# Kernel optimization log

Measured on AMD Instinct MI355X. Metric: run time of the kernel, lower is better.

The kernel has to match this reference:

```python
import jax, jax.numpy as jnp
import numpy as np

# Config (matches init_kwargs)
B, DIM = 16, 768
HEADS, DHEAD = 12, 64
H_MEM, W_MEM = 16, 16           # memory grid; N = 256 tokens
MAX_AH, MAX_AW = 3, 3
N = H_MEM * W_MEM


def _area_pool(t):
    """t: [B', N, D] laid out on an H_MEM x W_MEM grid.
    Returns (area_sums [B', M, D], area_sizes [M]) over all rectangle sizes
    (ah, aw) with 1<=ah<=MAX_AH, 1<=aw<=MAX_AW, at every valid position,
    via a 2D integral image (summed-area table)."""
    Bp, _, D = t.shape
    g = t.reshape(Bp, H_MEM, W_MEM, D)
    I = jnp.cumsum(jnp.cumsum(g, axis=1), axis=2)
    I = jnp.pad(I, ((0, 0), (1, 0), (1, 0), (0, 0)))  # [B', H+1, W+1, D]
    sums, sizes = [], []
    for ah in range(1, MAX_AH + 1):
        for aw in range(1, MAX_AW + 1):
            s = (I[:, ah:, aw:] - I[:, :-ah, aw:]
                 - I[:, ah:, :-aw] + I[:, :-ah, :-aw])  # [B', H-ah+1, W-aw+1, D]
            n_pos = s.shape[1] * s.shape[2]
            sums.append(s.reshape(Bp, n_pos, D))
            sizes.append(np.full((n_pos,), float(ah * aw), dtype=np.float32))
    return jnp.concatenate(sums, axis=1), jnp.asarray(np.concatenate(sizes))


def setup_inputs() -> dict:
    key = jax.random.key(0)
    ks = jax.random.split(key, 10)
    s = 0.02
    d = dict(
        x=jax.random.normal(ks[0], (B, N, DIM), jnp.float32),
        # to_qkv: Linear(dim, 3*dim, bias=False); stored as (in, out)
        w_qkv=jax.random.normal(ks[1], (DIM, 3 * DIM), jnp.float32) * s,
        # per-head q/k/v projections (dim -> heads*dim_head) with bias
        w_q=jax.random.normal(ks[2], (DIM, HEADS * DHEAD), jnp.float32) * s,
        b_q=jnp.zeros((HEADS * DHEAD,), jnp.float32),
        w_k=jax.random.normal(ks[3], (DIM, HEADS * DHEAD), jnp.float32) * s,
        b_k=jnp.zeros((HEADS * DHEAD,), jnp.float32),
        w_v=jax.random.normal(ks[4], (DIM, HEADS * DHEAD), jnp.float32) * s,
        b_v=jnp.zeros((HEADS * DHEAD,), jnp.float32),
        # output projection (heads*dim_head -> dim)
        w_o=jax.random.normal(ks[5], (HEADS * DHEAD, DIM), jnp.float32) * s,
        b_o=jnp.zeros((DIM,), jnp.float32),
    )
    return d


def reference(x, w_qkv, w_q, b_q, w_k, b_k, w_v, b_v, w_o, b_o):
    # QKV projection + split: 'b n (qkv d) -> qkv b n d'
    qkv = x @ w_qkv                               # [B, N, 3*DIM]
    q, k, v = jnp.split(qkv, 3, axis=-1)          # each [B, N, DIM]

    def to_heads(t, w, b):                        # 'b n (h d) -> (b h) n d'
        return ((t @ w + b)
                .reshape(B, N, HEADS, DHEAD)
                .transpose(0, 2, 1, 3)
                .reshape(B * HEADS, N, DHEAD))

    qh = to_heads(q, w_q, b_q)
    kh = to_heads(k, w_k, b_k)
    vh = to_heads(v, w_v, b_v)

    # Area keys: mean over each area; area values: sum over each area.
    k_sum, sizes = _area_pool(kh)                 # [BH, M, d], [M]
    k_area = k_sum / sizes[None, :, None]
    v_area, _ = _area_pool(vh)                    # [BH, M, d]

    logits = jnp.einsum('bqd,bmd->bqm', qh, k_area)   # [BH, N, M]
    weights = jax.nn.softmax(logits, axis=-1)
    out = jnp.einsum('bqm,bmd->bqd', weights, v_area)  # [BH, N, d]

    # '(b h) n d -> b n (h d)' then output projection
    out = (out.reshape(B, HEADS, N, DHEAD)
              .transpose(0, 2, 1, 3)
              .reshape(B, N, HEADS * DHEAD))
    return out @ w_o + b_o
```

## Files before the change

kernel.cpp:

```cpp
#include <hip/hip_runtime.h>
#include <hip/hip_bf16.h>

typedef __hip_bfloat16 bf16;
typedef __attribute__((ext_vector_type(8))) short short8b;
typedef __attribute__((ext_vector_type(4))) short short4b;
typedef __attribute__((ext_vector_type(4))) float f32x4;

#define NAREA 2025
#define NAREA_PAD 2048

static __device__ __forceinline__ float b2f(bf16 x) { return __bfloat162float(x); }
static __device__ __forceinline__ short f2bs(float f) {
  bf16 h = __float2bfloat16(f);
  return *(short*)&h;
}

static __device__ __forceinline__ void gll16(const void* g, void* l) {
  __builtin_amdgcn_global_load_lds(
      (const __attribute__((address_space(1))) unsigned int*)(unsigned long long)g,
      (__attribute__((address_space(3))) unsigned int*)(unsigned int)(unsigned long long)l,
      16, 0, 0);
}

__global__ __launch_bounds__(256) void k_prep(
    const float* __restrict__ x, const float* __restrict__ wqkv,
    const float* __restrict__ wq, const float* __restrict__ wk,
    const float* __restrict__ wv,
    bf16* __restrict__ xb, bf16* __restrict__ wqkvb,
    bf16* __restrict__ wqT, bf16* __restrict__ wkT, bf16* __restrict__ wvT,
    int4* __restrict__ rectG, float* __restrict__ invG)
{
  __shared__ float tile[32][33];
  int b = blockIdx.x;
  if (b < 4800) {
    int idx = (b * 256 + threadIdx.x) * 4;
    const int NX = 4096 * 768;
    float4 v;
    bf16* d;
    if (idx < NX) { v = *(const float4*)(x + idx); d = xb + idx; }
    else { v = *(const float4*)(wqkv + (idx - NX)); d = wqkvb + (idx - NX); }
    short4b s = {f2bs(v.x), f2bs(v.y), f2bs(v.z), f2bs(v.w)};
    *(short4b*)d = s;
    return;
  }
  if (b < 6528) {
    int r = b - 4800;
    int z = r / 576; r -= z * 576;
    int by = r / 24, bx = r - by * 24;
    const float* src = (z == 0) ? wq : (z == 1) ? wk : wv;
    bf16* dst = (z == 0) ? wqT : (z == 1) ? wkT : wvT;
    int r0 = by * 32, c0 = bx * 32;
    int lx = threadIdx.x & 31, ly = threadIdx.x >> 5;
#pragma unroll
    for (int yy = 0; yy < 4; ++yy)
      tile[ly + yy * 8][lx] = src[(size_t)(r0 + ly + yy * 8) * 768 + c0 + lx];
    __syncthreads();
#pragma unroll
    for (int yy = 0; yy < 4; ++yy)
      dst[(size_t)(c0 + ly + yy * 8) * 768 + r0 + lx] =
          __float2bfloat16(tile[lx][ly + yy * 8]);
    return;
  }
  int m = (b - 6528) * 256 + threadIdx.x;
  if (m >= NAREA_PAD) return;
  int4 rc = make_int4(0, 0, 0, 0);
  float iv = 0.f;
  if (m < NAREA) {
    int rem = m, ah = 1, aw = 1, found = 0;
    for (int a = 1; a <= 3 && !found; ++a)
      for (int w = 1; w <= 3 && !found; ++w) {
        int np = (17 - a) * (17 - w);
        if (rem < np) { ah = a; aw = w; found = 1; }
        else rem -= np;
      }
    int cw = 17 - aw;
    int y = rem / cw, xx = rem - y * cw;
    rc.x = (y * 17 + xx) * 64;
    rc.y = (y * 17 + (xx + aw)) * 64;
    rc.z = ((y + ah) * 17 + xx) * 64;
    rc.w = ((y + ah) * 17 + (xx + aw)) * 64;
    iv = 1.0f / (float)(ah * aw);
  }
  rectG[m] = rc;
  invG[m] = iv;
}

__global__ __launch_bounds__(256) void k_tcast1(
    const float* __restrict__ src, bf16* __restrict__ dst)
{
  __shared__ float tile[32][33];
  int r0 = blockIdx.y * 32, c0 = blockIdx.x * 32;
  int lx = threadIdx.x & 31, ly = threadIdx.x >> 5;
#pragma unroll
  for (int yy = 0; yy < 4; ++yy)
    tile[ly + yy * 8][lx] = src[(size_t)(r0 + ly + yy * 8) * 768 + c0 + lx];
  __syncthreads();
#pragma unroll
  for (int yy = 0; yy < 4; ++yy)
    dst[(size_t)(c0 + ly + yy * 8) * 768 + r0 + lx] =
        __float2bfloat16(tile[lx][ly + yy * 8]);
}


__global__ __launch_bounds__(256) void k_combine_m(
    const bf16* __restrict__ wqkvb, const bf16* __restrict__ wqT,
    const bf16* __restrict__ wkT, const bf16* __restrict__ wvT,
    bf16* __restrict__ WcTb)
{
  __shared__ __align__(16) short As[2][128 * 32];
  __shared__ __align__(16) short Bs[2][128 * 32];
  const int t3 = blockIdx.z;
  const bf16* BT = (t3 == 0) ? wqT : (t3 == 1) ? wkT : wvT;
  const int m0 = blockIdx.y * 128, n0 = blockIdx.x * 128;
  const int tid = threadIdx.x, lane = tid & 63, w = tid >> 6;
  const int tt = lane & 15, q4 = lane >> 4;
  const int moff = (w & 1) * 64, noff = (w >> 1) * 64;
  const int r_a = tid >> 2, kc = (tid & 3) * 8;

  f32x4 acc[4][4];
#pragma unroll
  for (int i = 0; i < 4; ++i)
#pragma unroll
    for (int j = 0; j < 4; ++j) acc[i][j] = (f32x4){0.f, 0.f, 0.f, 0.f};

#define STAGE_C(k0, buf)                                                        \
  {                                                                             \
    gll16(wqkvb + (size_t)(m0 + r_a) * 2304 + t3 * 768 + (k0) + kc,             \
          &As[buf][w * 512]);                                                   \
    gll16(wqkvb + (size_t)(m0 + r_a + 64) * 2304 + t3 * 768 + (k0) + kc,        \
          &As[buf][2048 + w * 512]);                                            \
    gll16(BT + (size_t)(n0 + r_a) * 768 + (k0) + kc, &Bs[buf][w * 512]);        \
    gll16(BT + (size_t)(n0 + r_a + 64) * 768 + (k0) + kc,                       \
          &Bs[buf][2048 + w * 512]);                                            \
  }

  STAGE_C(0, 0);
  for (int it = 0; it < 24; ++it) {
    __syncthreads();
    if (it < 23) STAGE_C((it + 1) * 32, (it + 1) & 1);
    const short* as = As[it & 1];
    const short* bs = Bs[it & 1];
    short8b afr[4], bfr[4];
#pragma unroll
    for (int mt = 0; mt < 4; ++mt)
      afr[mt] = *(const short8b*)&as[(moff + mt * 16 + tt) * 32 + q4 * 8];
#pragma unroll
    for (int nt = 0; nt < 4; ++nt)
      bfr[nt] = *(const short8b*)&bs[(noff + nt * 16 + tt) * 32 + q4 * 8];
#pragma unroll
    for (int mt = 0; mt < 4; ++mt)
#pragma unroll
      for (int nt = 0; nt < 4; ++nt)
        acc[mt][nt] = __builtin_amdgcn_mfma_f32_16x16x32_bf16(afr[mt], bfr[nt], acc[mt][nt], 0, 0, 0);
  }
#undef STAGE_C

  bf16* C = WcTb + (size_t)t3 * 768 * 768;
#pragma unroll
  for (int nt = 0; nt < 4; ++nt) {
    int n = n0 + noff + nt * 16 + tt;
#pragma unroll
    for (int mt = 0; mt < 4; ++mt) {
      int mb = m0 + moff + mt * 16 + q4 * 4;
      short4b v = {f2bs(acc[mt][nt][0]), f2bs(acc[mt][nt][1]),
                   f2bs(acc[mt][nt][2]), f2bs(acc[mt][nt][3])};
      *(short4b*)&C[(size_t)n * 768 + mb] = v;
    }
  }
}

__global__ __launch_bounds__(256) void k_proj_m(
    const bf16* __restrict__ xb, const bf16* __restrict__ WcTb,
    const float* __restrict__ bq, const float* __restrict__ bk,
    const float* __restrict__ bv,
    bf16* __restrict__ qh, bf16* __restrict__ kh, bf16* __restrict__ vh)
{
  __shared__ __align__(16) short As[2][128 * 32];
  __shared__ __align__(16) short Bs[2][128 * 32];
  const int t3 = blockIdx.z;
  const bf16* BT = WcTb + (size_t)t3 * 768 * 768;
  const float* bias = (t3 == 0) ? bq : (t3 == 1) ? bk : bv;
  bf16* dst = (t3 == 0) ? qh : (t3 == 1) ? kh : vh;
  const int m0 = blockIdx.y * 128, n0 = blockIdx.x * 128;
  const int tid = threadIdx.x, lane = tid & 63, w = tid >> 6;
  const int tt = lane & 15, q4 = lane >> 4;
  const int moff = (w & 1) * 64, noff = (w >> 1) * 64;
  const int r_a = tid >> 2, kc = (tid & 3) * 8;

  f32x4 acc[4][4];
#pragma unroll
  for (int i = 0; i < 4; ++i)
#pragma unroll
    for (int j = 0; j < 4; ++j) acc[i][j] = (f32x4){0.f, 0.f, 0.f, 0.f};

#define STAGE_P(k0, buf)                                                        \
  {                                                                             \
    gll16(xb + (size_t)(m0 + r_a) * 768 + (k0) + kc, &As[buf][w * 512]);        \
    gll16(xb + (size_t)(m0 + r_a + 64) * 768 + (k0) + kc,                       \
          &As[buf][2048 + w * 512]);                                            \
    gll16(BT + (size_t)(n0 + r_a) * 768 + (k0) + kc, &Bs[buf][w * 512]);        \
    gll16(BT + (size_t)(n0 + r_a + 64) * 768 + (k0) + kc,                       \
          &Bs[buf][2048 + w * 512]);                                            \
  }

  STAGE_P(0, 0);
  for (int it = 0; it < 24; ++it) {
    __syncthreads();
    if (it < 23) STAGE_P((it + 1) * 32, (it + 1) & 1);
    const short* as = As[it & 1];
    const short* bs = Bs[it & 1];
    short8b afr[4], bfr[4];
#pragma unroll
    for (int mt = 0; mt < 4; ++mt)
      afr[mt] = *(const short8b*)&as[(moff + mt * 16 + tt) * 32 + q4 * 8];
#pragma unroll
    for (int nt = 0; nt < 4; ++nt)
      bfr[nt] = *(const short8b*)&bs[(noff + nt * 16 + tt) * 32 + q4 * 8];
#pragma unroll
    for (int mt = 0; mt < 4; ++mt)
#pragma unroll
      for (int nt = 0; nt < 4; ++nt)
        acc[mt][nt] = __builtin_amdgcn_mfma_f32_16x16x32_bf16(afr[mt], bfr[nt], acc[mt][nt], 0, 0, 0);
  }
#undef STAGE_P

#pragma unroll
  for (int nt = 0; nt < 4; ++nt) {
    int c = n0 + noff + nt * 16 + tt;
    float bvv = bias[c];
    int h = c >> 6, d = c & 63;
#pragma unroll
    for (int mt = 0; mt < 4; ++mt) {
#pragma unroll
      for (int r = 0; r < 4; ++r) {
        int m = m0 + moff + mt * 16 + q4 * 4 + r;
        dst[(((size_t)((m >> 8) * 12 + h)) << 14) + ((m & 255) << 6) + d] =
            __float2bfloat16(acc[mt][nt][r] + bvv);
      }
    }
  }
}

__global__ __launch_bounds__(256) void k_out_m(
    const bf16* __restrict__ attno, const bf16* __restrict__ woT,
    const float* __restrict__ bo, float* __restrict__ out)
{
  __shared__ __align__(16) short As[2][128 * 32];
  __shared__ __align__(16) short Bs[2][128 * 32];
  const int m0 = blockIdx.y * 128, n0 = blockIdx.x * 128;
  const int tid = threadIdx.x, lane = tid & 63, w = tid >> 6;
  const int tt = lane & 15, q4 = lane >> 4;
  const int moff = (w & 1) * 64, noff = (w >> 1) * 64;
  const int r_a = tid >> 2, kc = (tid & 3) * 8;
  const int m_a0 = m0 + r_a, m_a1 = m0 + r_a + 64;

  f32x4 acc[4][4];
#pragma unroll
  for (int i = 0; i < 4; ++i)
#pragma unroll
    for (int j = 0; j < 4; ++j) acc[i][j] = (f32x4){0.f, 0.f, 0.f, 0.f};

#define STAGE_O(k0, buf)                                                        \
  {                                                                             \
    int k = (k0) + kc;                                                          \
    gll16(attno + (((size_t)((m_a0 >> 8) * 12 + (k >> 6))) << 14) +             \
              ((m_a0 & 255) << 6) + (k & 63),                                   \
          &As[buf][w * 512]);                                                   \
    gll16(attno + (((size_t)((m_a1 >> 8) * 12 + (k >> 6))) << 14) +             \
              ((m_a1 & 255) << 6) + (k & 63),                                   \
          &As[buf][2048 + w * 512]);                                            \
    gll16(woT + (size_t)(n0 + r_a) * 768 + k, &Bs[buf][w * 512]);               \
    gll16(woT + (size_t)(n0 + r_a + 64) * 768 + k, &Bs[buf][2048 + w * 512]);   \
  }

  STAGE_O(0, 0);
  for (int it = 0; it < 24; ++it) {
    __syncthreads();
    if (it < 23) STAGE_O((it + 1) * 32, (it + 1) & 1);
    const short* as = As[it & 1];
    const short* bs = Bs[it & 1];
    short8b afr[4], bfr[4];
#pragma unroll
    for (int mt = 0; mt < 4; ++mt)
      afr[mt] = *(const short8b*)&as[(moff + mt * 16 + tt) * 32 + q4 * 8];
#pragma unroll
    for (int nt = 0; nt < 4; ++nt)
      bfr[nt] = *(const short8b*)&bs[(noff + nt * 16 + tt) * 32 + q4 * 8];
#pragma unroll
    for (int mt = 0; mt < 4; ++mt)
#pragma unroll
      for (int nt = 0; nt < 4; ++nt)
        acc[mt][nt] = __builtin_amdgcn_mfma_f32_16x16x32_bf16(afr[mt], bfr[nt], acc[mt][nt], 0, 0, 0);
  }
#undef STAGE_O

#pragma unroll
  for (int nt = 0; nt < 4; ++nt) {
    int c = n0 + noff + nt * 16 + tt;
    float bvv = bo[c];
#pragma unroll
    for (int mt = 0; mt < 4; ++mt)
#pragma unroll
      for (int r = 0; r < 4; ++r) {
        int m = m0 + moff + mt * 16 + q4 * 4 + r;
        out[(size_t)m * 768 + c] = acc[mt][nt][r] + bvv;
      }
  }
}

__global__ __launch_bounds__(1024) void k_area_pre(
    const bf16* __restrict__ kh, const bf16* __restrict__ vh,
    const int4* __restrict__ rectG, const float* __restrict__ invG,
    bf16* __restrict__ Karea, bf16* __restrict__ VareaT)
{
  __shared__ float sat[17 * 17 * 65];
  int bh = blockIdx.x >> 1;
  bool isv = blockIdx.x & 1;
  const bf16* src = (isv ? vh : kh) + ((size_t)bh << 14);
  int tid = threadIdx.x;
  int d = tid & 63;
  int row = tid >> 6;
  {
    float run = 0.f;
    sat[((row + 1) * 17) * 65 + d] = 0.f;
#pragma unroll
    for (int xx = 0; xx < 16; ++xx) {
      run += b2f(src[(row * 16 + xx) * 64 + d]);
      sat[((row + 1) * 17 + (xx + 1)) * 65 + d] = run;
    }
    if (row == 0) {
#pragma unroll
      for (int xx = 0; xx < 17; ++xx) sat[xx * 65 + d] = 0.f;
    }
  }
  __syncthreads();
  {
    int x = row + 1;
    float run = 0.f;
#pragma unroll
    for (int y = 1; y <= 16; ++y) {
      run += sat[(y * 17 + x) * 65 + d];
      sat[(y * 17 + x) * 65 + d] = run;
    }
  }
  __syncthreads();
  if (!isv) {
    int mrow = tid >> 3;
    int d0 = (tid & 7) * 8;
    bf16* out = Karea + ((size_t)bh << 17);
    for (int s = 0; s < 16; ++s) {
      int m = s * 128 + mrow;
      int4 rc = rectG[m];
      int cx = rc.x + (rc.x >> 6), cy = rc.y + (rc.y >> 6);
      int cz = rc.z + (rc.z >> 6), cw = rc.w + (rc.w >> 6);
      float iv = invG[m];
      short v[8];
#pragma unroll
      for (int j = 0; j < 8; ++j) {
        int dd = d0 + j;
        float df = sat[cw + dd] - sat[cy + dd] - sat[cz + dd] + sat[cx + dd];
        v[j] = f2bs(df * iv);
      }
      *(short8b*)&out[((size_t)m << 6) + d0] =
          (short8b){v[0], v[1], v[2], v[3], v[4], v[5], v[6], v[7]};
    }
  } else {
    int mcol = tid & 63;
    int r16 = tid >> 6;
    bf16* out = VareaT + ((size_t)bh << 17);
    for (int s = 0; s < 128; ++s) {
      int idx = s * 16 + r16;
      int it = idx >> 6, dd = idx & 63;
      int4 rc = rectG[it * 64 + mcol];
      int cx = rc.x + (rc.x >> 6), cy = rc.y + (rc.y >> 6);
      int cz = rc.z + (rc.z >> 6), cw = rc.w + (rc.w >> 6);
      float df = sat[cw + dd] - sat[cy + dd] - sat[cz + dd] + sat[cx + dd];
      out[(((size_t)it << 6) + dd) * 64 + mcol] = __float2bfloat16(df);
    }
  }
}

__global__ __launch_bounds__(256, 4) void k_attn_f(
    const bf16* __restrict__ qh, const bf16* __restrict__ Karea,
    const bf16* __restrict__ VareaT, bf16* __restrict__ attno)
{
  __shared__ __align__(16) short aK2[2][64 * 80];
  __shared__ __align__(16) short aVt2[2][64 * 80];

  const int tid = threadIdx.x;
  const int lane = tid & 63;
  const int w = tid >> 6;
  const int t = lane & 15;
  const int q4 = lane >> 4;
  const int bh = blockIdx.x;
  const int Q0 = blockIdx.y * 128;
  const int rbase = (t & 12) * 2 + (t & 3);

  const bf16* Kb = Karea + ((size_t)bh << 17);
  const bf16* Vb = VareaT + ((size_t)bh << 17);
  const bf16* qrowA = qh + ((size_t)bh << 14) + (size_t)(Q0 + w * 32 + t) * 64;
  const bf16* qrowB = qrowA + 16 * 64;

  short8b qfA0 = *(const short8b*)(qrowA + q4 * 8);
  short8b qfA1 = *(const short8b*)(qrowA + 32 + q4 * 8);
  short8b qfB0 = *(const short8b*)(qrowB + q4 * 8);
  short8b qfB1 = *(const short8b*)(qrowB + 32 + q4 * 8);

  f32x4 OA[4], OB[4];
#pragma unroll
  for (int i = 0; i < 4; ++i) {
    OA[i] = (f32x4){0.f, 0.f, 0.f, 0.f};
    OB[i] = (f32x4){0.f, 0.f, 0.f, 0.f};
  }
  float lA = 0.f, lB = 0.f;

  const int a8 = tid >> 2;
  const int c8 = (tid & 3) * 16;

  {
    short8b k0a = *(const short8b*)&Kb[((size_t)a8 << 6) + c8];
    short8b k0b = *(const short8b*)&Kb[((size_t)a8 << 6) + c8 + 8];
    short8b v0a = *(const short8b*)&Vb[((size_t)a8 << 6) + c8];
    short8b v0b = *(const short8b*)&Vb[((size_t)a8 << 6) + c8 + 8];
    *(short8b*)&aK2[0][a8 * 80 + c8] = k0a;
    *(short8b*)&aK2[0][a8 * 80 + c8 + 8] = k0b;
    *(short8b*)&aVt2[0][a8 * 80 + c8] = v0a;
    *(short8b*)&aVt2[0][a8 * 80 + c8 + 8] = v0b;
  }

  for (int it = 0; it < 32; ++it) {
    short8b kna, knb, vna, vnb;
    if (it + 1 < 32) {
      size_t off = ((size_t)((it + 1) * 64 + a8) << 6) + c8;
      kna = *(const short8b*)&Kb[off];
      knb = *(const short8b*)&Kb[off + 8];
      vna = *(const short8b*)&Vb[off];
      vnb = *(const short8b*)&Vb[off + 8];
    }
    __syncthreads();
    const short* aK = aK2[it & 1];
    const short* aVt = aVt2[it & 1];
    if (it + 1 < 32) {
      short* aKn = aK2[(it + 1) & 1];
      short* aVtn = aVt2[(it + 1) & 1];
      *(short8b*)&aKn[a8 * 80 + c8] = kna;
      *(short8b*)&aKn[a8 * 80 + c8 + 8] = knb;
      *(short8b*)&aVtn[a8 * 80 + c8] = vna;
      *(short8b*)&aVtn[a8 * 80 + c8 + 8] = vnb;
    }

    const int t0 = it * 64;
    const bool edge = (t0 + 64 > NAREA);
    union { short8b v; unsigned u[4]; } apvA[2], apvB[2];
#pragma unroll
    for (int at = 0; at < 4; ++at) {
      int row = rbase + (at & 1) * 4 + (at >> 1) * 32;
      short8b af0 = *(const short8b*)&aK[row * 80 + q4 * 8];
      short8b af1 = *(const short8b*)&aK[row * 80 + 32 + q4 * 8];
      int abase = t0 + (at >> 1) * 32 + q4 * 8 + (at & 1) * 4;
      {
        f32x4 s = (f32x4){0.f, 0.f, 0.f, 0.f};
        s = __builtin_amdgcn_mfma_f32_16x16x32_bf16(af0, qfA0, s, 0, 0, 0);
        s = __builtin_amdgcn_mfma_f32_16x16x32_bf16(af1, qfA1, s, 0, 0, 0);
        float p[4];
#pragma unroll
        for (int r = 0; r < 4; ++r) {
          p[r] = __expf(s[r]);
          if (edge && (abase + r >= NAREA)) p[r] = 0.f;
        }
        lA += (p[0] + p[1]) + (p[2] + p[3]);
        unsigned lo = ((unsigned)(unsigned short)f2bs(p[1]) << 16) |
                      (unsigned short)f2bs(p[0]);
        unsigned hi = ((unsigned)(unsigned short)f2bs(p[3]) << 16) |
                      (unsigned short)f2bs(p[2]);
        apvA[at >> 1].u[(at & 1) * 2 + 0] = lo;
        apvA[at >> 1].u[(at & 1) * 2 + 1] = hi;
      }
      {
        f32x4 s = (f32x4){0.f, 0.f, 0.f, 0.f};
        s = __builtin_amdgcn_mfma_f32_16x16x32_bf16(af0, qfB0, s, 0, 0, 0);
        s = __builtin_amdgcn_mfma_f32_16x16x32_bf16(af1, qfB1, s, 0, 0, 0);
        float p[4];
#pragma unroll
        for (int r = 0; r < 4; ++r) {
          p[r] = __expf(s[r]);
          if (edge && (abase + r >= NAREA)) p[r] = 0.f;
        }
        lB += (p[0] + p[1]) + (p[2] + p[3]);
        unsigned lo = ((unsigned)(unsigned short)f2bs(p[1]) << 16) |
                      (unsigned short)f2bs(p[0]);
        unsigned hi = ((unsigned)(unsigned short)f2bs(p[3]) << 16) |
                      (unsigned short)f2bs(p[2]);
        apvB[at >> 1].u[(at & 1) * 2 + 0] = lo;
        apvB[at >> 1].u[(at & 1) * 2 + 1] = hi;
      }
    }
#pragma unroll
    for (int nt = 0; nt < 4; ++nt) {
      short8b vf0 = *(const short8b*)&aVt[(nt * 16 + t) * 80 + q4 * 8];
      short8b vf1 = *(const short8b*)&aVt[(nt * 16 + t) * 80 + 32 + q4 * 8];
      OA[nt] = __builtin_amdgcn_mfma_f32_16x16x32_bf16(apvA[0].v, vf0, OA[nt], 0, 0, 0);
      OA[nt] = __builtin_amdgcn_mfma_f32_16x16x32_bf16(apvA[1].v, vf1, OA[nt], 0, 0, 0);
      OB[nt] = __builtin_amdgcn_mfma_f32_16x16x32_bf16(apvB[0].v, vf0, OB[nt], 0, 0, 0);
      OB[nt] = __builtin_amdgcn_mfma_f32_16x16x32_bf16(apvB[1].v, vf1, OB[nt], 0, 0, 0);
    }
  }

  lA += __shfl_xor(lA, 16, 64);
  lA += __shfl_xor(lA, 32, 64);
  lB += __shfl_xor(lB, 16, 64);
  lB += __shfl_xor(lB, 32, 64);

  bf16* ob = attno + ((size_t)bh << 14);
#pragma unroll
  for (int r = 0; r < 4; ++r) {
    int qr = q4 * 4 + r;
    float invlA = 1.0f / __shfl(lA, qr, 64);
    float invlB = 1.0f / __shfl(lB, qr, 64);
    int baseA = (Q0 + w * 32 + qr) * 64;
    int baseB = baseA + 16 * 64;
#pragma unroll
    for (int nt = 0; nt < 4; ++nt) {
      ob[baseA + nt * 16 + t] = __float2bfloat16(OA[nt][r] * invlA);
      ob[baseB + nt * 16 + t] = __float2bfloat16(OB[nt][r] * invlB);
    }
  }
}

__global__ __launch_bounds__(1024) void k_integral_p(
    const bf16* __restrict__ kh, const bf16* __restrict__ vh,
    float* __restrict__ Ik, float* __restrict__ Iv)
{
  __shared__ float sat[17 * 17 * 64];
  int bh = blockIdx.x >> 1;
  bool isv = blockIdx.x & 1;
  const bf16* src = (isv ? vh : kh) + ((size_t)bh << 14);
  float* dst = (isv ? Iv : Ik) + (size_t)bh * 18496;
  int tid = threadIdx.x;
  int d = tid & 63;
  int row = tid >> 6;
  {
    float run = 0.f;
    sat[((row + 1) * 17) * 64 + d] = 0.f;
#pragma unroll
    for (int xx = 0; xx < 16; ++xx) {
      run += b2f(src[(row * 16 + xx) * 64 + d]);
      sat[((row + 1) * 17 + (xx + 1)) * 64 + d] = run;
    }
    if (row == 0) {
#pragma unroll
      for (int xx = 0; xx < 17; ++xx) sat[xx * 64 + d] = 0.f;
    }
  }
  __syncthreads();
  {
    int x = row + 1;
    float run = 0.f;
#pragma unroll
    for (int y = 1; y <= 16; ++y) {
      run += sat[(y * 17 + x) * 64 + d];
      sat[(y * 17 + x) * 64 + d] = run;
    }
  }
  __syncthreads();
  for (int i = tid; i < 18496; i += 1024) dst[i] = sat[i];
}

__global__ __launch_bounds__(1024) void k_attn_m(
    const bf16* __restrict__ qh, const float* __restrict__ Ik,
    const float* __restrict__ Iv, const int4* __restrict__ rectG,
    const float* __restrict__ invG, bf16* __restrict__ attno)
{
  __shared__ __align__(16) short aK2[2][64 * 80];
  __shared__ __align__(16) short aVt2[2][64 * 72];

  const int tid = threadIdx.x;
  const int lane = tid & 63;
  const int w = tid >> 6;
  const int t = lane & 15;
  const int q4 = lane >> 4;
  const int bh = blockIdx.x;
  const int rbase = (t & 12) * 2 + (t & 3);

  const float* Ikb = Ik + (size_t)bh * 18496;
  const float* Ivb = Iv + (size_t)bh * 18496;
  const bf16* qbase = qh + ((size_t)bh << 14);

  short8b qf0 = *(const short8b*)(qbase + (w * 16 + t) * 64 + q4 * 8);
  short8b qf1 = *(const short8b*)(qbase + (w * 16 + t) * 64 + 32 + q4 * 8);

  f32x4 O[4];
#pragma unroll
  for (int i = 0; i < 4; ++i) O[i] = (f32x4){0.f, 0.f, 0.f, 0.f};
  float l = 0.f;

  {
    short* aK = aK2[0];
    short* aVt = aVt2[0];
    short vp[4];
#pragma unroll
    for (int i = 0; i < 4; ++i) {
      int j = w * 4 + i;
      int4 rc = rectG[j];
      float iv = invG[j];
      float kc = Ikb[rc.w + lane] - Ikb[rc.y + lane] - Ikb[rc.z + lane] + Ikb[rc.x + lane];
      float vc = Ivb[rc.w + lane] - Ivb[rc.y + lane] - Ivb[rc.z + lane] + Ivb[rc.x + lane];
      aK[j * 80 + lane] = f2bs(kc * iv);
      vp[i] = f2bs(vc);
    }
    *(short4b*)&aVt[lane * 72 + w * 4] = (short4b){vp[0], vp[1], vp[2], vp[3]};
  }

  float kcr[4], vcr[4], ivr[4];
  for (int it = 0; it < 32; ++it) {
    if (it + 1 < 32) {
      int t0n = (it + 1) * 64;
#pragma unroll
      for (int i = 0; i < 4; ++i) {
        int j = t0n + w * 4 + i;
        int4 rc = rectG[j];
        ivr[i] = invG[j];
        kcr[i] = Ikb[rc.w + lane] - Ikb[rc.y + lane] - Ikb[rc.z + lane] + Ikb[rc.x + lane];
        vcr[i] = Ivb[rc.w + lane] - Ivb[rc.y + lane] - Ivb[rc.z + lane] + Ivb[rc.x + lane];
      }
    }
    __syncthreads();
    const short* aK = aK2[it & 1];
    const short* aVt = aVt2[it & 1];
    if (it + 1 < 32) {
      short* aKn = aK2[(it + 1) & 1];
      short* aVtn = aVt2[(it + 1) & 1];
      short vp[4];
#pragma unroll
      for (int i = 0; i < 4; ++i) {
        aKn[(w * 4 + i) * 80 + lane] = f2bs(kcr[i] * ivr[i]);
        vp[i] = f2bs(vcr[i]);
      }
      *(short4b*)&aVtn[lane * 72 + w * 4] = (short4b){vp[0], vp[1], vp[2], vp[3]};
    }

    const int t0 = it * 64;
    const bool edge = (t0 + 64 > NAREA);
    union { short8b v; unsigned u[4]; } apv[2];
#pragma unroll
    for (int at = 0; at < 4; ++at) {
      int row = rbase + (at & 1) * 4 + (at >> 1) * 32;
      short8b af0 = *(const short8b*)&aK[row * 80 + q4 * 8];
      short8b af1 = *(const short8b*)&aK[row * 80 + 32 + q4 * 8];
      f32x4 s = (f32x4){0.f, 0.f, 0.f, 0.f};
      s = __builtin_amdgcn_mfma_f32_16x16x32_bf16(af0, qf0, s, 0, 0, 0);
      s = __builtin_amdgcn_mfma_f32_16x16x32_bf16(af1, qf1, s, 0, 0, 0);
      int abase = t0 + (at >> 1) * 32 + q4 * 8 + (at & 1) * 4;
      float p[4];
#pragma unroll
      for (int r = 0; r < 4; ++r) {
        p[r] = __expf(s[r]);
        if (edge && (abase + r >= NAREA)) p[r] = 0.f;
      }
      l += (p[0] + p[1]) + (p[2] + p[3]);
      unsigned lo = ((unsigned)(unsigned short)f2bs(p[1]) << 16) |
                    (unsigned short)f2bs(p[0]);
      unsigned hi = ((unsigned)(unsigned short)f2bs(p[3]) << 16) |
                    (unsigned short)f2bs(p[2]);
      apv[at >> 1].u[(at & 1) * 2 + 0] = lo;
      apv[at >> 1].u[(at & 1) * 2 + 1] = hi;
    }
#pragma unroll
    for (int nt = 0; nt < 4; ++nt) {
      short8b vf0 = *(const short8b*)&aVt[(nt * 16 + t) * 72 + q4 * 8];
      short8b vf1 = *(const short8b*)&aVt[(nt * 16 + t) * 72 + 32 + q4 * 8];
      O[nt] = __builtin_amdgcn_mfma_f32_16x16x32_bf16(apv[0].v, vf0, O[nt], 0, 0, 0);
      O[nt] = __builtin_amdgcn_mfma_f32_16x16x32_bf16(apv[1].v, vf1, O[nt], 0, 0, 0);
    }
  }

  l += __shfl_xor(l, 16, 64);
  l += __shfl_xor(l, 32, 64);

  bf16* ob = attno + ((size_t)bh << 14);
#pragma unroll
  for (int r = 0; r < 4; ++r) {
    int qrow = q4 * 4 + r;
    float invl = 1.0f / __shfl(l, qrow, 64);
#pragma unroll
    for (int nt = 0; nt < 4; ++nt)
      ob[(w * 16 + qrow) * 64 + nt * 16 + t] = __float2bfloat16(O[nt][r] * invl);
  }
}

extern "C" void kernel_launch(void* const* d_in, const int* in_sizes, int n_in,
                              void* d_out, int out_size, void* d_ws, size_t ws_size,
                              hipStream_t stream) {
  const float* x    = (const float*)d_in[0];
  const float* wqkv = (const float*)d_in[1];
  const float* wq   = (const float*)d_in[2];
  const float* bq   = (const float*)d_in[3];
  const float* wk   = (const float*)d_in[4];
  const float* bk   = (const float*)d_in[5];
  const float* wv   = (const float*)d_in[6];
  const float* bv   = (const float*)d_in[7];
  const float* wo   = (const float*)d_in[8];
  const float* bo   = (const float*)d_in[9];
  float* out = (float*)d_out;

  char* ws = (char*)d_ws;
  char* ob = (char*)d_out;
  const size_t WC_B = 7077888;
  const size_t QH_B = 6291456;
  const size_t AREA_B = 50331648;

  bf16* xb    = (bf16*)ob;
  bf16* WcTb  = (bf16*)(ob + QH_B);
  bf16* attno = (bf16*)ws;
  int4*  rectG = (int4*)(ws + QH_B);
  float* invG  = (float*)(ws + QH_B + 32768);
  bf16* qh = (bf16*)(ws + WC_B);
  bf16* kh = (bf16*)(ws + WC_B + QH_B);
  bf16* vh = (bf16*)(ws + WC_B + 2 * QH_B);
  bf16* wqkvb = (bf16*)(ws + WC_B);
  bf16* wqT   = (bf16*)(ws + WC_B + 3538944);
  bf16* wkT   = (bf16*)(ws + WC_B + 4718592);
  bf16* wvT   = (bf16*)(ws + WC_B + 5898240);
  bf16* Karea  = (bf16*)(ws + WC_B + 3 * QH_B);
  bf16* VareaT = (bf16*)(ws + WC_B + 3 * QH_B + AREA_B);
  float* Ik = (float*)(ws + WC_B + 3 * QH_B);
  float* Iv = Ik + 3551232;
  bf16* woT = (bf16*)(ws + WC_B + 3 * QH_B);

  const size_t REQ = WC_B + 3 * QH_B + 2 * AREA_B;
  const bool primary = (ws_size >= REQ);

  k_prep<<<dim3(6536), 256, 0, stream>>>(x, wqkv, wq, wk, wv, xb, wqkvb,
                                         wqT, wkT, wvT, rectG, invG);
  k_combine_m<<<dim3(6, 6, 3), 256, 0, stream>>>(wqkvb, wqT, wkT, wvT, WcTb);
  k_proj_m<<<dim3(6, 32, 3), 256, 0, stream>>>(xb, WcTb, bq, bk, bv, qh, kh, vh);
  if (primary) {
    k_area_pre<<<dim3(384), 1024, 0, stream>>>(kh, vh, rectG, invG, Karea, VareaT);
    k_attn_f<<<dim3(192, 2), 256, 0, stream>>>(qh, Karea, VareaT, attno);
  } else {
    k_integral_p<<<dim3(384), 1024, 0, stream>>>(kh, vh, Ik, Iv);
    k_attn_m<<<dim3(192), 1024, 0, stream>>>(qh, Ik, Iv, rectG, invG, attno);
  }
  k_tcast1<<<dim3(24, 24), 256, 0, stream>>>(wo, woT);
  k_out_m<<<dim3(6, 32), 256, 0, stream>>>(attno, woT, bo, out);
}
```

Measured before the change: 237.4 us.

## Split attention over area dimension into two halves and vectorize V-area transpose stores

After: 315.2 us. 32.8% more time.

```diff
diff --git a/kernel.cpp b/kernel.cpp
--- a/kernel.cpp
+++ b/kernel.cpp
@@ -365,35 +365,42 @@
           (short8b){v[0], v[1], v[2], v[3], v[4], v[5], v[6], v[7]};
     }
   } else {
-    int mcol = tid & 63;
-    int r16 = tid >> 6;
+    int m8 = (tid & 7) * 8;
     bf16* out = VareaT + ((size_t)bh << 17);
-    for (int s = 0; s < 128; ++s) {
-      int idx = s * 16 + r16;
+    for (int s = 0; s < 16; ++s) {
+      int idx = s * 128 + (tid >> 3);
       int it = idx >> 6, dd = idx & 63;
-      int4 rc = rectG[it * 64 + mcol];
-      int cx = rc.x + (rc.x >> 6), cy = rc.y + (rc.y >> 6);
-      int cz = rc.z + (rc.z >> 6), cw = rc.w + (rc.w >> 6);
-      float df = sat[cw + dd] - sat[cy + dd] - sat[cz + dd] + sat[cx + dd];
-      out[(((size_t)it << 6) + dd) * 64 + mcol] = __float2bfloat16(df);
-    }
-  }
-}
-
-__global__ __launch_bounds__(256, 4) void k_attn_f(
+      short v[8];
+#pragma unroll
+      for (int j = 0; j < 8; ++j) {
+        int4 rc = rectG[it * 64 + m8 + j];
+        int cx = rc.x + (rc.x >> 6), cy = rc.y + (rc.y >> 6);
+        int cz = rc.z + (rc.z >> 6), cw = rc.w + (rc.w >> 6);
+        v[j] = f2bs(sat[cw + dd] - sat[cy + dd] - sat[cz + dd] + sat[cx + dd]);
+      }
+      *(short8b*)&out[(((size_t)it << 6) + dd) * 64 + m8] =
+          (short8b){v[0], v[1], v[2], v[3], v[4], v[5], v[6], v[7]};
+    }
+  }
+}
+
+__global__ __launch_bounds__(256, 4) void k_attn_g(
     const bf16* __restrict__ qh, const bf16* __restrict__ Karea,
-    const bf16* __restrict__ VareaT, bf16* __restrict__ attno)
+    const bf16* __restrict__ VareaT,
+    float* __restrict__ Op0, float* __restrict__ Op1,
+    float* __restrict__ lp0, float* __restrict__ lp1)
 {
   __shared__ __align__(16) short aK2[2][64 * 80];
   __shared__ __align__(16) short aVt2[2][64 * 80];
 
   const int tid = threadIdx.x;
+  const int w = tid >> 6;
   const int lane = tid & 63;
-  const int w = tid >> 6;
   const int t = lane & 15;
   const int q4 = lane >> 4;
   const int bh = blockIdx.x;
   const int Q0 = blockIdx.y * 128;
+  const int it0 = blockIdx.z * 16;
   const int rbase = (t & 12) * 2 + (t & 3);
 
   const bf16* Kb = Karea + ((size_t)bh << 17);
@@ -418,19 +425,20 @@
   const int c8 = (tid & 3) * 16;
 
   {
-    short8b k0a = *(const short8b*)&Kb[((size_t)a8 << 6) + c8];
-    short8b k0b = *(const short8b*)&Kb[((size_t)a8 << 6) + c8 + 8];
-    short8b v0a = *(const short8b*)&Vb[((size_t)a8 << 6) + c8];
-    short8b v0b = *(const short8b*)&Vb[((size_t)a8 << 6) + c8 + 8];
+    size_t off = ((size_t)(it0 * 64 + a8) << 6) + c8;
+    short8b k0a = *(const short8b*)&Kb[off];
+    short8b k0b = *(const short8b*)&Kb[off + 8];
+    short8b v0a = *(const short8b*)&Vb[off];
+    short8b v0b = *(const short8b*)&Vb[off + 8];
     *(short8b*)&aK2[0][a8 * 80 + c8] = k0a;
     *(short8b*)&aK2[0][a8 * 80 + c8 + 8] = k0b;
     *(short8b*)&aVt2[0][a8 * 80 + c8] = v0a;
     *(short8b*)&aVt2[0][a8 * 80 + c8 + 8] = v0b;
   }
 
-  for (int it = 0; it < 32; ++it) {
+  for (int it = it0; it < it0 + 16; ++it) {
     short8b kna, knb, vna, vnb;
-    if (it + 1 < 32) {
+    if (it + 1 < it0 + 16) {
       size_t off = ((size_t)((it + 1) * 64 + a8) << 6) + c8;
       kna = *(const short8b*)&Kb[off];
       knb = *(const short8b*)&Kb[off + 8];
@@ -440,7 +448,7 @@
     __syncthreads();
     const short* aK = aK2[it & 1];
     const short* aVt = aVt2[it & 1];
-    if (it + 1 < 32) {
+    if (it + 1 < it0 + 16) {
       short* aKn = aK2[(it + 1) & 1];
       short* aVtn = aVt2[(it + 1) & 1];
       *(short8b*)&aKn[a8 * 80 + c8] = kna;
@@ -511,20 +519,37 @@
   lB += __shfl_xor(lB, 16, 64);
   lB += __shfl_xor(lB, 32, 64);
 
-  bf16* ob = attno + ((size_t)bh << 14);
+  float* lp = blockIdx.z ? lp1 : lp0;
+  float* Op = blockIdx.z ? Op1 : Op0;
+  if (q4 == 0) {
+    lp[(bh << 8) + Q0 + w * 32 + t] = lA;
+    lp[(bh << 8) + Q0 + w * 32 + 16 + t] = lB;
+  }
+  float* Ob = Op + (((size_t)(bh << 8) + Q0 + w * 32) << 6);
 #pragma unroll
   for (int r = 0; r < 4; ++r) {
     int qr = q4 * 4 + r;
-    float invlA = 1.0f / __shfl(lA, qr, 64);
-    float invlB = 1.0f / __shfl(lB, qr, 64);
-    int baseA = (Q0 + w * 32 + qr) * 64;
-    int baseB = baseA + 16 * 64;
 #pragma unroll
     for (int nt = 0; nt < 4; ++nt) {
-      ob[baseA + nt * 16 + t] = __float2bfloat16(OA[nt][r] * invlA);
-      ob[baseB + nt * 16 + t] = __float2bfloat16(OB[nt][r] * invlB);
-    }
-  }
+      Ob[qr * 64 + nt * 16 + t] = OA[nt][r];
+      Ob[(16 + qr) * 64 + nt * 16 + t] = OB[nt][r];
+    }
+  }
+}
+
+__global__ __launch_bounds__(256) void k_norm2(
+    const float* __restrict__ Op0, const float* __restrict__ Op1,
+    const float* __restrict__ lp0, const float* __restrict__ lp1,
+    bf16* __restrict__ attno)
+{
+  int i = (blockIdx.x * 256 + threadIdx.x) * 4;
+  f32x4 a = *(const f32x4*)(Op0 + i);
+  f32x4 b = *(const f32x4*)(Op1 + i);
+  int q = i >> 6;
+  float invl = 1.0f / (lp0[q] + lp1[q]);
+  short4b s = {f2bs((a[0] + b[0]) * invl), f2bs((a[1] + b[1]) * invl),
+               f2bs((a[2] + b[2]) * invl), f2bs((a[3] + b[3]) * invl)};
+  *(short4b*)(attno + i) = s;
 }
 
 __global__ __launch_bounds__(1024) void k_integral_p(
@@ -711,12 +736,16 @@
 
   bf16* xb    = (bf16*)ob;
   bf16* WcTb  = (bf16*)(ob + QH_B);
+  float* Op0  = (float*)ob;
   bf16* attno = (bf16*)ws;
   int4*  rectG = (int4*)(ws + QH_B);
   float* invG  = (float*)(ws + QH_B + 32768);
+  float* lp0   = (float*)(ws + QH_B + 40960);
+  float* lp1   = lp0 + 49152;
   bf16* qh = (bf16*)(ws + WC_B);
   bf16* kh = (bf16*)(ws + WC_B + QH_B);
   bf16* vh = (bf16*)(ws + WC_B + 2 * QH_B);
+  float* Op1 = (float*)(ws + WC_B + QH_B);
   bf16* wqkvb = (bf16*)(ws + WC_B);
   bf16* wqT   = (bf16*)(ws + WC_B + 3538944);
   bf16* wkT   = (bf16*)(ws + WC_B + 4718592);
@@ -736,7 +765,9 @@
   k_proj_m<<<dim3(6, 32, 3), 256, 0, stream>>>(xb, WcTb, bq, bk, bv, qh, kh, vh);
   if (primary) {
     k_area_pre<<<dim3(384), 1024, 0, stream>>>(kh, vh, rectG, invG, Karea, VareaT);
-    k_attn_f<<<dim3(192, 2), 256, 0, stream>>>(qh, Karea, VareaT, attno);
+    k_attn_g<<<dim3(192, 2, 2), 256, 0, stream>>>(qh, Karea, VareaT,
+                                                  Op0, Op1, lp0, lp1);
+    k_norm2<<<dim3(3072), 256, 0, stream>>>(Op0, Op1, lp0, lp1, attno);
   } else {
     k_integral_p<<<dim3(384), 1024, 0, stream>>>(kh, vh, Ik, Iv);
     k_attn_m<<<dim3(192), 1024, 0, stream>>>(qh, Ik, Iv, rectG, invG, attno);
```
